# Performance work log

Measured on AMD Instinct MI355X. Metric: run time of the kernel, lower is better.

## Reference

```python
import jax, jax.numpy as jnp
import numpy as np


def setup_inputs() -> dict:
    key = jax.random.key(0)
    k_x, k_m, k_wq, k_wk, k_bq, k_bk = jax.random.split(key, 6)
    B, L, D, P = 8, 2048, 128, 64
    x = jax.random.normal(k_x, (B, L, D), dtype=jnp.float32)
    padding_mask = jax.random.randint(k_m, (B, L), 0, 2).astype(bool)
    lim = 1.0 / np.sqrt(D)
    Wq = jax.random.uniform(k_wq, (D, P), jnp.float32, -lim, lim)
    Wk = jax.random.uniform(k_wk, (D, P), jnp.float32, -lim, lim)
    bq = jax.random.uniform(k_bq, (P,), jnp.float32, -lim, lim)
    bk = jax.random.uniform(k_bk, (P,), jnp.float32, -lim, lim)
    return {"x": x, "padding_mask": padding_mask, "Wq": Wq, "bq": bq,
            "Wk": Wk, "bk": bk, "top_k": 64}


def reference(x, padding_mask, Wq, bq, Wk, bk, top_k):
    B, L, _ = x.shape
    P = Wq.shape[1]
    scale = jnp.asarray(P, x.dtype) ** 0.5
    Q = x @ Wq + bq                      # (B, L, P)
    K = x @ Wk + bk                      # (B, L, P)
    scores = jnp.einsum('blp,bmp->blm', Q, K) / scale   # (B, L, L)
    # valid pair mask: keep (i, j) only if both positions are unpadded
    full_mask = padding_mask[:, :, None] & padding_mask[:, None, :]
    flat = jnp.where(full_mask.reshape(B, L * L),
                     scores.reshape(B, L * L), -jnp.inf)
    topk_vals, topk_idx = jax.lax.top_k(flat, top_k)     # (B, K)
    topk_weights = jax.nn.softmax(topk_vals, axis=-1)
    topk_indices = jnp.stack([topk_idx // L, topk_idx % L], axis=-1)  # (B, K, 2)
    return topk_indices, topk_weights
```

## Files before the change

kernel.cpp:

```cpp
#include <hip/hip_runtime.h>
#include <float.h>
#include <limits.h>
#include <math.h>

namespace {

constexpr int NB = 8;
constexpr int SL = 2048;
constexpr int DIM = 128;
constexpr int PP = 64;
constexpr int KK = 64;
constexpr int ROWS = 128;
constexpr int CTILE = 128;
constexpr int NSTRIP = SL / ROWS;
constexpr int CSPLIT = 4;
constexpr int NSLOT = NSTRIP * CSPLIT;
constexpr int CAP = 512;
constexpr int PROJ_ROWS = 32;
constexpr int NPROJ = NB * SL / PROJ_ROWS;
constexpr float MARGIN = 4e-3f;

__device__ __forceinline__ bool cgt64(double v1, int i1, double v2, int i2) {
  return (v1 > v2) || (v1 == v2 && i1 < i2);
}
__device__ __forceinline__ bool cgt32(float v1, int i1, float v2, int i2) {
  return (v1 > v2) || (v1 == v2 && i1 < i2);
}

__global__ __launch_bounds__(256) void proj_compact_kernel(
    const float* __restrict__ x, const void* __restrict__ mask_raw,
    const float* __restrict__ Wq, const float* __restrict__ bq,
    const float* __restrict__ Wk, const float* __restrict__ bk,
    float* __restrict__ Q, float* __restrict__ K,
    int* __restrict__ pos, int* __restrict__ cnt) {
  const int tid = threadIdx.x;
  if (blockIdx.x >= NPROJ) {
    const int b = blockIdx.x - NPROJ;
    const int lane = tid & 63, wid = tid >> 6;
    __shared__ int bytemode;
    __shared__ int wsum[4];
    if (tid == 0) bytemode = 0;
    __syncthreads();
    const unsigned char* allb = (const unsigned char*)mask_raw;
    int local = 0;
    for (int t = tid; t < 512; t += 256)
      if ((t & 3) != 0 && allb[t] != 0) local = 1;
    if (local) atomicOr(&bytemode, 1);
    __syncthreads();
    int f[8]; int c = 0;
    const int base = tid * 8;
    if (bytemode) {
      const unsigned char* p = allb + (size_t)b * SL;
      for (int j = 0; j < 8; ++j) { f[j] = p[base + j] ? 1 : 0; c += f[j]; }
    } else {
      const int* p = (const int*)mask_raw + (size_t)b * SL;
      for (int j = 0; j < 8; ++j) { f[j] = p[base + j] ? 1 : 0; c += f[j]; }
    }
    int incl = c;
    for (int off = 1; off < 64; off <<= 1) {
      int t = __shfl_up(incl, off);
      if (lane >= off) incl += t;
    }
    if (lane == 63) wsum[wid] = incl;
    __syncthreads();
    int woff = 0;
    for (int w = 0; w < wid; ++w) woff += wsum[w];
    int k = woff + incl - c;
    for (int j = 0; j < 8; ++j)
      if (f[j]) pos[b * SL + (k++)] = base + j;
    if (tid == 255) cnt[b] = k;
    return;
  }
  __shared__ __align__(16) float sx[PROJ_ROWS * DIM];
  const int row0 = blockIdx.x * PROJ_ROWS;
  for (int t = tid; t < PROJ_ROWS * 32; t += 256) {
    const int row = t >> 5, f = t & 31;
    *(float4*)&sx[row * DIM + f * 4] =
        *(const float4*)(x + (size_t)(row0 + row) * DIM + f * 4);
  }
  __syncthreads();
  const int rq = tid >> 5;
  const int pp = (tid & 31) * 2;
  double aq[4][2] = {}, cq[4][2] = {}, ak[4][2] = {}, ck[4][2] = {};
  for (int d = 0; d < DIM; d += 4) {
    float4 xv[4];
#pragma unroll
    for (int i = 0; i < 4; ++i)
      xv[i] = *(const float4*)&sx[(rq * 4 + i) * DIM + d];
    const float2 wq0 = *(const float2*)&Wq[(d + 0) * PP + pp];
    const float2 wq1 = *(const float2*)&Wq[(d + 1) * PP + pp];
    const float2 wq2 = *(const float2*)&Wq[(d + 2) * PP + pp];
    const float2 wq3 = *(const float2*)&Wq[(d + 3) * PP + pp];
    const float2 wk0 = *(const float2*)&Wk[(d + 0) * PP + pp];
    const float2 wk1 = *(const float2*)&Wk[(d + 1) * PP + pp];
    const float2 wk2 = *(const float2*)&Wk[(d + 2) * PP + pp];
    const float2 wk3 = *(const float2*)&Wk[(d + 3) * PP + pp];
#pragma unroll
    for (int i = 0; i < 4; ++i) {
      const double x0 = (double)xv[i].x, x1 = (double)xv[i].y;
      const double x2 = (double)xv[i].z, x3 = (double)xv[i].w;
      aq[i][0] += x0 * (double)wq0.x; aq[i][1] += x0 * (double)wq0.y;
      cq[i][0] += x1 * (double)wq1.x; cq[i][1] += x1 * (double)wq1.y;
      aq[i][0] += x2 * (double)wq2.x; aq[i][1] += x2 * (double)wq2.y;
      cq[i][0] += x3 * (double)wq3.x; cq[i][1] += x3 * (double)wq3.y;
      ak[i][0] += x0 * (double)wk0.x; ak[i][1] += x0 * (double)wk0.y;
      ck[i][0] += x1 * (double)wk1.x; ck[i][1] += x1 * (double)wk1.y;
      ak[i][0] += x2 * (double)wk2.x; ak[i][1] += x2 * (double)wk2.y;
      ck[i][0] += x3 * (double)wk3.x; ck[i][1] += x3 * (double)wk3.y;
    }
  }
  const double b0q = (double)bq[pp], b1q = (double)bq[pp + 1];
  const double b0k = (double)bk[pp], b1k = (double)bk[pp + 1];
#pragma unroll
  for (int i = 0; i < 4; ++i) {
    const size_t o = ((size_t)row0 + rq * 4 + i) * PP + pp;
    Q[o]     = (float)(aq[i][0] + cq[i][0] + b0q);
    Q[o + 1] = (float)(aq[i][1] + cq[i][1] + b1q);
    K[o]     = (float)(ak[i][0] + ck[i][0] + b0k);
    K[o + 1] = (float)(ak[i][1] + ck[i][1] + b1k);
  }
}

__global__ __launch_bounds__(256, 2) void score_kernel(
    const float* __restrict__ Q, const float* __restrict__ K,
    const int* __restrict__ pos, const int* __restrict__ cnt,
    double* __restrict__ chunk_val, int* __restrict__ chunk_idx) {
  __shared__ __align__(16) float sQ[128 * 68];
  __shared__ __align__(16) float sK[128 * 68];
  __shared__ float cval[CAP];
  __shared__ int cidx[CAP];
  __shared__ float smax[256];
  __shared__ int spos_r[ROWS], spos_c[CTILE];
  __shared__ int cnt_sh, ovf, mcnt;
  __shared__ float thresh;

  const int b = blockIdx.y, strip = blockIdx.z, colq = blockIdx.x;
  const int tid = threadIdx.x, lane = tid & 63;
  const int nv = cnt[b];
  const int slot = (b * NSTRIP + strip) * CSPLIT + colq;
  const int r0 = strip * ROWS;
  const int per = (nv + CSPLIT - 1) / CSPLIT;
  const int cbeg = colq * per;
  const int cend = min(cbeg + per, nv);
  double* chv = chunk_val + (size_t)slot * KK;
  int* chi = chunk_idx + (size_t)slot * KK;
  if (r0 >= nv || cbeg >= cend) {
    if (tid < KK) { chv[tid] = -DBL_MAX; chi[tid] = INT_MAX; }
    return;
  }
  const int nrows = min(ROWS, nv - r0);
  if (tid < ROWS) spos_r[tid] = (tid < nrows) ? pos[b * SL + r0 + tid] : 0;
  for (int t = tid; t < 128 * 16; t += 256) {
    const int row = t >> 4, p4 = t & 15;
    float4 v = make_float4(0.f, 0.f, 0.f, 0.f);
    if (row < nrows) {
      const int g = pos[b * SL + r0 + row];
      v = *(const float4*)(Q + ((size_t)b * SL + g) * PP + p4 * 4);
    }
    *(float4*)&sQ[row * 68 + p4 * 4] = v;
  }
  if (tid == 0) { cnt_sh = 0; ovf = 0; thresh = -FLT_MAX; }
  __syncthreads();

  const int ry = tid & 15, cy = tid >> 4;

  for (int c0 = cbeg; c0 < cend; c0 += CTILE) {
    const int ncols = min(CTILE, cend - c0);
    if (tid < CTILE) spos_c[tid] = (tid < ncols) ? pos[b * SL + c0 + tid] : 0;
    for (int t = tid; t < 128 * 16; t += 256) {
      const int col = t >> 4, p4 = t & 15;
      float4 v = make_float4(0.f, 0.f, 0.f, 0.f);
      if (col < ncols) {
        const int g = pos[b * SL + c0 + col];
        v = *(const float4*)(K + ((size_t)b * SL + g) * PP + p4 * 4);
      }
      *(float4*)&sK[col * 68 + p4 * 4] = v;
    }
    __syncthreads();

    float acc[8][8] = {};
    for (int p4 = 0; p4 < 16; ++p4) {
      float4 qv[8], kv[8];
#pragma unroll
      for (int i = 0; i < 8; ++i) qv[i] = *(const float4*)&sQ[(ry + 16 * i) * 68 + p4 * 4];
#pragma unroll
      for (int j = 0; j < 8; ++j) kv[j] = *(const float4*)&sK[(cy + 16 * j) * 68 + p4 * 4];
#pragma unroll
      for (int i = 0; i < 8; ++i)
#pragma unroll
        for (int j = 0; j < 8; ++j) {
          acc[i][j] = fmaf(qv[i].x, kv[j].x, acc[i][j]);
          acc[i][j] = fmaf(qv[i].y, kv[j].y, acc[i][j]);
          acc[i][j] = fmaf(qv[i].z, kv[j].z, acc[i][j]);
          acc[i][j] = fmaf(qv[i].w, kv[j].w, acc[i][j]);
        }
    }

    if (c0 == cbeg) {
      float tmax = -FLT_MAX;
      for (int i = 0; i < 8; ++i) {
        const int rr = ry + 16 * i;
        if (rr >= nrows) continue;
        for (int j = 0; j < 8; ++j) {
          const int cc = cy + 16 * j;
          if (cc >= ncols) continue;
          tmax = fmaxf(tmax, acc[i][j] * 0.125f);
        }
      }
      smax[tid] = tmax;
      __syncthreads();
      for (int k2 = 2; k2 <= 256; k2 <<= 1)
        for (int j2 = k2 >> 1; j2 >= 1; j2 >>= 1) {
          if (tid < 128) {
            const int i = ((tid & ~(j2 - 1)) << 1) | (tid & (j2 - 1));
            const int p = i | j2;
            const bool desc = ((i & k2) == 0);
            const float vi = smax[i], vp = smax[p];
            const bool sw = desc ? (vp > vi) : (vi > vp);
            if (sw) { smax[i] = vp; smax[p] = vi; }
          }
          __syncthreads();
        }
      if (tid == 0 && smax[KK - 1] > -FLT_MAX) thresh = smax[KK - 1] - MARGIN;
      __syncthreads();
    }

    bool pushed = false;
    for (int attempt = 0; attempt < 8; ++attempt) {
      const float th = thresh;
      int nloc = 0;
      for (int i = 0; i < 8; ++i) {
        const int rr = ry + 16 * i;
        if (rr >= nrows) continue;
        for (int j = 0; j < 8; ++j) {
          const int cc = cy + 16 * j;
          if (cc >= ncols) continue;
          if (acc[i][j] * 0.125f >= th) nloc++;
        }
      }
      int incl = nloc;
      for (int off = 1; off < 64; off <<= 1) {
        int t2 = __shfl_up(incl, off);
        if (lane >= off) incl += t2;
      }
      const int wtot = __shfl(incl, 63);
      if (!pushed) {
        if (wtot == 0) {
          pushed = true;
        } else {
          int wbase = 0;
          if (lane == 63) {
            wbase = atomicAdd(&cnt_sh, wtot);
            if (wbase + wtot > CAP) { atomicAdd(&cnt_sh, -wtot); wbase = -1; ovf = 1; }
          }
          wbase = __shfl(wbase, 63);
          if (wbase >= 0) {
            int sl = wbase + incl - nloc;
            for (int i = 0; i < 8; ++i) {
              const int rr = ry + 16 * i;
              if (rr >= nrows) continue;
              for (int j = 0; j < 8; ++j) {
                const int cc = cy + 16 * j;
                if (cc >= ncols) continue;
                const float s = acc[i][j] * 0.125f;
                if (s >= th) {
                  cval[sl] = s;
                  cidx[sl] = spos_r[rr] * SL + spos_c[cc];
                  ++sl;
                }
              }
            }
            pushed = true;
          }
        }
      }
      __syncthreads();
      if (ovf == 0) break;
      {
        const int n = cnt_sh;
        for (int j = n + tid; j < CAP; j += 256) { cval[j] = -FLT_MAX; cidx[j] = INT_MAX; }
        __syncthreads();
        for (int k2 = 2; k2 <= CAP; k2 <<= 1)
          for (int j2 = k2 >> 1; j2 >= 1; j2 >>= 1) {
            const int i = ((tid & ~(j2 - 1)) << 1) | (tid & (j2 - 1));
            const int p = i | j2;
            const bool desc = ((i & k2) == 0);
            const float vi = cval[i], vp = cval[p];
            const int ii = cidx[i], ip = cidx[p];
            const bool sw = desc ? cgt32(vp, ip, vi, ii) : cgt32(vi, ii, vp, ip);
            if (sw) { cval[i] = vp; cidx[i] = ip; cval[p] = vi; cidx[p] = ii; }
            __syncthreads();
          }
        const float t64 = cval[KK - 1];
        const float nth = (t64 > -FLT_MAX) ? (t64 - MARGIN) : thresh;
        for (int j = tid; j < CAP; j += 256) {
          const bool in = (cidx[j] != INT_MAX) && (cval[j] >= nth);
          const bool nx = (j + 1 < CAP) && (cidx[j + 1] != INT_MAX) && (cval[j + 1] >= nth);
          if (in && !nx) mcnt = j + 1;
          if (j == 0 && !in) mcnt = 0;
        }
        __syncthreads();
        if (tid == 0) { thresh = nth; cnt_sh = mcnt; ovf = 0; }
        __syncthreads();
      }
    }
    __syncthreads();
  }

  const int n = cnt_sh;
  double* rval = (double*)sQ;
  for (int base2 = 0; base2 < n; base2 += 32) {
    const int s = base2 + (tid >> 3);
    double p = 0;
    if (s < n) {
      const int fi = cidx[s];
      const int orow = fi >> 11, ocol = fi & (SL - 1);
      const float* qr = Q + ((size_t)b * SL + orow) * PP + (tid & 7) * 8;
      const float* kr = K + ((size_t)b * SL + ocol) * PP + (tid & 7) * 8;
#pragma unroll
      for (int e = 0; e < 8; ++e) p = fma((double)qr[e], (double)kr[e], p);
    }
    p += __shfl_down(p, 4);
    p += __shfl_down(p, 2);
    p += __shfl_down(p, 1);
    if (((tid & 7) == 0) && s < n) rval[s] = p * 0.125;
  }
  int np2 = KK;
  while (np2 < n) np2 <<= 1;
  for (int j = n + tid; j < np2; j += 256) { rval[j] = -DBL_MAX; cidx[j] = INT_MAX; }
  __syncthreads();
  for (int k2 = 2; k2 <= np2; k2 <<= 1)
    for (int j2 = k2 >> 1; j2 >= 1; j2 >>= 1) {
      if (tid < (np2 >> 1)) {
        const int i = ((tid & ~(j2 - 1)) << 1) | (tid & (j2 - 1));
        const int p = i | j2;
        const bool desc = ((i & k2) == 0);
        const double vi = rval[i], vp = rval[p];
        const int ii = cidx[i], ip = cidx[p];
        const bool sw = desc ? cgt64(vp, ip, vi, ii) : cgt64(vi, ii, vp, ip);
        if (sw) { rval[i] = vp; cidx[i] = ip; rval[p] = vi; cidx[p] = ii; }
      }
      __syncthreads();
    }
  if (tid < KK) { chv[tid] = rval[tid]; chi[tid] = cidx[tid]; }
}

__global__ __launch_bounds__(256) void merge_kernel(
    const double* __restrict__ chunk_val, const int* __restrict__ chunk_idx,
    float* __restrict__ out) {
  __shared__ double sval[NSLOT * 16];
  __shared__ int sidx[NSLOT * 16];
  const int b = blockIdx.x, tid = threadIdx.x;
  const double* vb = chunk_val + (size_t)b * NSLOT * KK;
  const int* ib = chunk_idx + (size_t)b * NSLOT * KK;
  for (int t = tid; t < NSLOT * 16; t += 256) {
    const int list = t >> 4, e = t & 15;
    sval[t] = vb[list * KK + e];
    sidx[t] = ib[list * KK + e];
  }
  __syncthreads();
  if (tid < 64) {
    const int lane = tid;
    int hp = 0;
    double cur = sval[lane * 16];
    int curi = sidx[lane * 16];
    double myv = -DBL_MAX; int myi = INT_MAX;
    for (int k = 0; k < KK; ++k) {
      double bv = cur; int bi = curi; int bg = lane;
      for (int off2 = 32; off2 > 0; off2 >>= 1) {
        const double v2 = __shfl_down(bv, off2);
        const int i2 = __shfl_down(bi, off2);
        const int g2 = __shfl_down(bg, off2);
        if (cgt64(v2, i2, bv, bi)) { bv = v2; bi = i2; bg = g2; }
      }
      bv = __shfl(bv, 0); bi = __shfl(bi, 0); bg = __shfl(bg, 0);
      if (bg == lane) {
        const int h = ++hp;
        if (h < 16) { cur = sval[lane * 16 + h]; curi = sidx[lane * 16 + h]; }
        else if (h < KK) { cur = vb[lane * KK + h]; curi = ib[lane * KK + h]; }
        else { cur = -DBL_MAX; curi = INT_MAX; }
      }
      if (lane == k) { myv = bv; myi = bi; }
    }
    const double m = __shfl(myv, 0);
    double e = (myi == INT_MAX || myv == -DBL_MAX) ? 0.0 : exp(myv - m);
    double s = e;
    for (int off2 = 32; off2 > 0; off2 >>= 1) s += __shfl_down(s, off2);
    s = __shfl(s, 0);
    if (s <= 0.0) s = 1.0;
    const double w = e / s;
    int row = 0, col = 0;
    if (myi != INT_MAX) { row = myi >> 11; col = myi & (SL - 1); }
    float* oidx = out;
    float* owt = out + (size_t)NB * KK * 2;
    oidx[((size_t)b * KK + lane) * 2 + 0] = (float)row;
    oidx[((size_t)b * KK + lane) * 2 + 1] = (float)col;
    owt[(size_t)b * KK + lane] = (float)w;
  }
}

}

extern "C" void kernel_launch(void* const* d_in, const int* in_sizes, int n_in,
                              void* d_out, int out_size, void* d_ws, size_t ws_size,
                              hipStream_t stream) {
  const float* x = (const float*)d_in[0];
  const void* mask_raw = d_in[1];
  const float* Wq = (const float*)d_in[2];
  const float* bq = (const float*)d_in[3];
  const float* Wk = (const float*)d_in[4];
  const float* bk = (const float*)d_in[5];
  float* out = (float*)d_out;

  char* ws = (char*)d_ws;
  const size_t qk = (size_t)NB * SL * PP;
  float* Q = (float*)ws;
  float* K = (float*)(ws + qk * 4);
  size_t off = qk * 8;
  double* chunk_val = (double*)(ws + off); off += (size_t)NB * NSLOT * KK * 8;
  int* chunk_idx = (int*)(ws + off);       off += (size_t)NB * NSLOT * KK * 4;
  int* pos = (int*)(ws + off);             off += (size_t)NB * SL * 4;
  int* cntv = (int*)(ws + off);

  proj_compact_kernel<<<NPROJ + NB, 256, 0, stream>>>(
      x, mask_raw, Wq, bq, Wk, bk, Q, K, pos, cntv);
  score_kernel<<<dim3(CSPLIT, NB, NSTRIP), 256, 0, stream>>>(
      Q, K, pos, cntv, chunk_val, chunk_idx);
  merge_kernel<<<NB, 256, 0, stream>>>(chunk_val, chunk_idx, out);
}
```

Baseline: 191.9 us.

## Fuse projection, scoring and merge into one persistent kernel with atomic dependency counters

Merges the three kernel launches into a single launch whose block ranges play the projection, compaction, scoring and merge roles. Per-batch atomic counters with spin-waits replace the kernel boundaries, so scoring for one batch can start once that batch's projection is done, and the merge can start once its batch's scores are in. This removes launch gaps and lets stages overlap, at the cost of a memset launch, spin-wait polling, and a shared-memory union sized for the largest role, which may limit occupancy. Correctness relies on blocks being dispatched in index order so that the waiting blocks cannot starve the producers.

```diff
diff --git a/kernel.cpp b/kernel.cpp
--- a/kernel.cpp
+++ b/kernel.cpp
@@ -18,6 +18,8 @@
 constexpr int CAP = 512;
 constexpr int PROJ_ROWS = 32;
 constexpr int NPROJ = NB * SL / PROJ_ROWS;
+constexpr int NSCORE = CSPLIT * NB * NSTRIP;
+constexpr int PROJ_PER_BATCH = 64;
 constexpr float MARGIN = 4e-3f;
 
 __device__ __forceinline__ bool cgt64(double v1, int i1, double v2, int i2) {
@@ -27,29 +29,106 @@
   return (v1 > v2) || (v1 == v2 && i1 < i2);
 }
 
-__global__ __launch_bounds__(256) void proj_compact_kernel(
+union __align__(16) SMem {
+  struct {
+    float sQ[128 * 68];
+    float sK[128 * 68];
+    float cval[CAP];
+    int   cidx[CAP];
+    float smax[256];
+    int   spos_r[ROWS];
+    int   spos_c[CTILE];
+    int   cnt_sh, ovf, mcnt;
+    float thresh;
+  } sc;
+  struct { float sx[PROJ_ROWS * DIM]; } pj;
+  struct { int bytemode; int wsum[4]; } cp;
+  struct { double sval[NSLOT * 16]; int sidx[NSLOT * 16]; } mg;
+};
+
+__global__ __launch_bounds__(256, 2) void fused_kernel(
     const float* __restrict__ x, const void* __restrict__ mask_raw,
     const float* __restrict__ Wq, const float* __restrict__ bq,
     const float* __restrict__ Wk, const float* __restrict__ bk,
     float* __restrict__ Q, float* __restrict__ K,
-    int* __restrict__ pos, int* __restrict__ cnt) {
+    int* __restrict__ pos, int* __restrict__ cnt,
+    unsigned* __restrict__ ctr, unsigned* __restrict__ sdone,
+    double* __restrict__ chunk_val, int* __restrict__ chunk_idx,
+    float* __restrict__ out) {
+  __shared__ SMem sm;
+  const int bid = blockIdx.x;
   const int tid = threadIdx.x;
-  if (blockIdx.x >= NPROJ) {
-    const int b = blockIdx.x - NPROJ;
-    const int lane = tid & 63, wid = tid >> 6;
-    __shared__ int bytemode;
-    __shared__ int wsum[4];
-    if (tid == 0) bytemode = 0;
+  const int lane = tid & 63;
+
+  if (bid < NPROJ) {
+    float* sx = sm.pj.sx;
+    const int row0 = bid * PROJ_ROWS;
+    for (int t = tid; t < PROJ_ROWS * 32; t += 256) {
+      const int row = t >> 5, f = t & 31;
+      *(float4*)&sx[row * DIM + f * 4] =
+          *(const float4*)(x + (size_t)(row0 + row) * DIM + f * 4);
+    }
+    __syncthreads();
+    const int rq = tid >> 5;
+    const int pp = (tid & 31) * 2;
+    double aq[4][2] = {}, cq[4][2] = {}, ak[4][2] = {}, ck[4][2] = {};
+    for (int d = 0; d < DIM; d += 4) {
+      float4 xv[4];
+#pragma unroll
+      for (int i = 0; i < 4; ++i)
+        xv[i] = *(const float4*)&sx[(rq * 4 + i) * DIM + d];
+      const float2 wq0 = *(const float2*)&Wq[(d + 0) * PP + pp];
+      const float2 wq1 = *(const float2*)&Wq[(d + 1) * PP + pp];
+      const float2 wq2 = *(const float2*)&Wq[(d + 2) * PP + pp];
+      const float2 wq3 = *(const float2*)&Wq[(d + 3) * PP + pp];
+      const float2 wk0 = *(const float2*)&Wk[(d + 0) * PP + pp];
+      const float2 wk1 = *(const float2*)&Wk[(d + 1) * PP + pp];
+      const float2 wk2 = *(const float2*)&Wk[(d + 2) * PP + pp];
+      const float2 wk3 = *(const float2*)&Wk[(d + 3) * PP + pp];
+#pragma unroll
+      for (int i = 0; i < 4; ++i) {
+        const double x0 = (double)xv[i].x, x1 = (double)xv[i].y;
+        const double x2 = (double)xv[i].z, x3 = (double)xv[i].w;
+        aq[i][0] += x0 * (double)wq0.x; aq[i][1] += x0 * (double)wq0.y;
+        cq[i][0] += x1 * (double)wq1.x; cq[i][1] += x1 * (double)wq1.y;
+        aq[i][0] += x2 * (double)wq2.x; aq[i][1] += x2 * (double)wq2.y;
+        cq[i][0] += x3 * (double)wq3.x; cq[i][1] += x3 * (double)wq3.y;
+        ak[i][0] += x0 * (double)wk0.x; ak[i][1] += x0 * (double)wk0.y;
+        ck[i][0] += x1 * (double)wk1.x; ck[i][1] += x1 * (double)wk1.y;
+        ak[i][0] += x2 * (double)wk2.x; ak[i][1] += x2 * (double)wk2.y;
+        ck[i][0] += x3 * (double)wk3.x; ck[i][1] += x3 * (double)wk3.y;
+      }
+    }
+    const double b0q = (double)bq[pp], b1q = (double)bq[pp + 1];
+    const double b0k = (double)bk[pp], b1k = (double)bk[pp + 1];
+#pragma unroll
+    for (int i = 0; i < 4; ++i) {
+      const size_t o = ((size_t)row0 + rq * 4 + i) * PP + pp;
+      Q[o]     = (float)(aq[i][0] + cq[i][0] + b0q);
+      Q[o + 1] = (float)(aq[i][1] + cq[i][1] + b1q);
+      K[o]     = (float)(ak[i][0] + ck[i][0] + b0k);
+      K[o + 1] = (float)(ak[i][1] + ck[i][1] + b1k);
+    }
+    __threadfence();
+    __syncthreads();
+    if (tid == 0) atomicAdd(&ctr[bid >> 6], 1u);
+    return;
+  }
+
+  if (bid < NPROJ + NB) {
+    const int b = bid - NPROJ;
+    const int wid = tid >> 6;
+    if (tid == 0) sm.cp.bytemode = 0;
     __syncthreads();
     const unsigned char* allb = (const unsigned char*)mask_raw;
     int local = 0;
     for (int t = tid; t < 512; t += 256)
       if ((t & 3) != 0 && allb[t] != 0) local = 1;
-    if (local) atomicOr(&bytemode, 1);
+    if (local) atomicOr(&sm.cp.bytemode, 1);
     __syncthreads();
     int f[8]; int c = 0;
     const int base = tid * 8;
-    if (bytemode) {
+    if (sm.cp.bytemode) {
       const unsigned char* p = allb + (size_t)b * SL;
       for (int j = 0; j < 8; ++j) { f[j] = p[base + j] ? 1 : 0; c += f[j]; }
     } else {
@@ -61,341 +140,307 @@
       int t = __shfl_up(incl, off);
       if (lane >= off) incl += t;
     }
-    if (lane == 63) wsum[wid] = incl;
+    if (lane == 63) sm.cp.wsum[wid] = incl;
     __syncthreads();
     int woff = 0;
-    for (int w = 0; w < wid; ++w) woff += wsum[w];
+    for (int w = 0; w < wid; ++w) woff += sm.cp.wsum[w];
     int k = woff + incl - c;
     for (int j = 0; j < 8; ++j)
       if (f[j]) pos[b * SL + (k++)] = base + j;
     if (tid == 255) cnt[b] = k;
+    __threadfence();
+    __syncthreads();
+    if (tid == 0) atomicAdd(&ctr[b], 1u);
     return;
   }
-  __shared__ __align__(16) float sx[PROJ_ROWS * DIM];
-  const int row0 = blockIdx.x * PROJ_ROWS;
-  for (int t = tid; t < PROJ_ROWS * 32; t += 256) {
-    const int row = t >> 5, f = t & 31;
-    *(float4*)&sx[row * DIM + f * 4] =
-        *(const float4*)(x + (size_t)(row0 + row) * DIM + f * 4);
-  }
-  __syncthreads();
-  const int rq = tid >> 5;
-  const int pp = (tid & 31) * 2;
-  double aq[4][2] = {}, cq[4][2] = {}, ak[4][2] = {}, ck[4][2] = {};
-  for (int d = 0; d < DIM; d += 4) {
-    float4 xv[4];
-#pragma unroll
-    for (int i = 0; i < 4; ++i)
-      xv[i] = *(const float4*)&sx[(rq * 4 + i) * DIM + d];
-    const float2 wq0 = *(const float2*)&Wq[(d + 0) * PP + pp];
-    const float2 wq1 = *(const float2*)&Wq[(d + 1) * PP + pp];
-    const float2 wq2 = *(const float2*)&Wq[(d + 2) * PP + pp];
-    const float2 wq3 = *(const float2*)&Wq[(d + 3) * PP + pp];
-    const float2 wk0 = *(const float2*)&Wk[(d + 0) * PP + pp];
-    const float2 wk1 = *(const float2*)&Wk[(d + 1) * PP + pp];
-    const float2 wk2 = *(const float2*)&Wk[(d + 2) * PP + pp];
-    const float2 wk3 = *(const float2*)&Wk[(d + 3) * PP + pp];
-#pragma unroll
-    for (int i = 0; i < 4; ++i) {
-      const double x0 = (double)xv[i].x, x1 = (double)xv[i].y;
-      const double x2 = (double)xv[i].z, x3 = (double)xv[i].w;
-      aq[i][0] += x0 * (double)wq0.x; aq[i][1] += x0 * (double)wq0.y;
-      cq[i][0] += x1 * (double)wq1.x; cq[i][1] += x1 * (double)wq1.y;
-      aq[i][0] += x2 * (double)wq2.x; aq[i][1] += x2 * (double)wq2.y;
-      cq[i][0] += x3 * (double)wq3.x; cq[i][1] += x3 * (double)wq3.y;
-      ak[i][0] += x0 * (double)wk0.x; ak[i][1] += x0 * (double)wk0.y;
-      ck[i][0] += x1 * (double)wk1.x; ck[i][1] += x1 * (double)wk1.y;
-      ak[i][0] += x2 * (double)wk2.x; ak[i][1] += x2 * (double)wk2.y;
-      ck[i][0] += x3 * (double)wk3.x; ck[i][1] += x3 * (double)wk3.y;
-    }
-  }
-  const double b0q = (double)bq[pp], b1q = (double)bq[pp + 1];
-  const double b0k = (double)bk[pp], b1k = (double)bk[pp + 1];
-#pragma unroll
-  for (int i = 0; i < 4; ++i) {
-    const size_t o = ((size_t)row0 + rq * 4 + i) * PP + pp;
-    Q[o]     = (float)(aq[i][0] + cq[i][0] + b0q);
-    Q[o + 1] = (float)(aq[i][1] + cq[i][1] + b1q);
-    K[o]     = (float)(ak[i][0] + ck[i][0] + b0k);
-    K[o + 1] = (float)(ak[i][1] + ck[i][1] + b1k);
-  }
-}
-
-__global__ __launch_bounds__(256, 2) void score_kernel(
-    const float* __restrict__ Q, const float* __restrict__ K,
-    const int* __restrict__ pos, const int* __restrict__ cnt,
-    double* __restrict__ chunk_val, int* __restrict__ chunk_idx) {
-  __shared__ __align__(16) float sQ[128 * 68];
-  __shared__ __align__(16) float sK[128 * 68];
-  __shared__ float cval[CAP];
-  __shared__ int cidx[CAP];
-  __shared__ float smax[256];
-  __shared__ int spos_r[ROWS], spos_c[CTILE];
-  __shared__ int cnt_sh, ovf, mcnt;
-  __shared__ float thresh;
-
-  const int b = blockIdx.y, strip = blockIdx.z, colq = blockIdx.x;
-  const int tid = threadIdx.x, lane = tid & 63;
-  const int nv = cnt[b];
-  const int slot = (b * NSTRIP + strip) * CSPLIT + colq;
-  const int r0 = strip * ROWS;
-  const int per = (nv + CSPLIT - 1) / CSPLIT;
-  const int cbeg = colq * per;
-  const int cend = min(cbeg + per, nv);
-  double* chv = chunk_val + (size_t)slot * KK;
-  int* chi = chunk_idx + (size_t)slot * KK;
-  if (r0 >= nv || cbeg >= cend) {
-    if (tid < KK) { chv[tid] = -DBL_MAX; chi[tid] = INT_MAX; }
+
+  if (bid < NPROJ + NB + NSCORE) {
+    const int sid = bid - (NPROJ + NB);
+    const int colq = sid & 3;
+    const int b = (sid >> 2) & 7;
+    const int strip = sid >> 5;
+
+    if (tid == 0) {
+      while (atomicAdd(&ctr[b], 0u) < (unsigned)(PROJ_PER_BATCH + 1))
+        __builtin_amdgcn_s_sleep(8);
+    }
+    __syncthreads();
+    __threadfence();
+
+    float* sQ = sm.sc.sQ;
+    float* sK = sm.sc.sK;
+    const int nv = cnt[b];
+    const int slot = (b * NSTRIP + strip) * CSPLIT + colq;
+    const int r0 = strip * ROWS;
+    const int per = (nv + CSPLIT - 1) / CSPLIT;
+    const int cbeg = colq * per;
+    const int cend = min(cbeg + per, nv);
+    double* chv = chunk_val + (size_t)slot * KK;
+    int* chi = chunk_idx + (size_t)slot * KK;
+    if (r0 >= nv || cbeg >= cend) {
+      if (tid < KK) { chv[tid] = -DBL_MAX; chi[tid] = INT_MAX; }
+      __threadfence();
+      __syncthreads();
+      if (tid == 0) atomicAdd(&sdone[b], 1u);
+      return;
+    }
+    const int nrows = min(ROWS, nv - r0);
+    if (tid < ROWS) sm.sc.spos_r[tid] = (tid < nrows) ? pos[b * SL + r0 + tid] : 0;
+    for (int t = tid; t < 128 * 16; t += 256) {
+      const int row = t >> 4, p4 = t & 15;
+      float4 v = make_float4(0.f, 0.f, 0.f, 0.f);
+      if (row < nrows) {
+        const int g = pos[b * SL + r0 + row];
+        v = *(const float4*)(Q + ((size_t)b * SL + g) * PP + p4 * 4);
+      }
+      *(float4*)&sQ[row * 68 + p4 * 4] = v;
+    }
+    if (tid == 0) { sm.sc.cnt_sh = 0; sm.sc.ovf = 0; sm.sc.thresh = -FLT_MAX; }
+    __syncthreads();
+
+    const int ry = tid & 15, cy = tid >> 4;
+
+    for (int c0 = cbeg; c0 < cend; c0 += CTILE) {
+      const int ncols = min(CTILE, cend - c0);
+      if (tid < CTILE) sm.sc.spos_c[tid] = (tid < ncols) ? pos[b * SL + c0 + tid] : 0;
+      for (int t = tid; t < 128 * 16; t += 256) {
+        const int col = t >> 4, p4 = t & 15;
+        float4 v = make_float4(0.f, 0.f, 0.f, 0.f);
+        if (col < ncols) {
+          const int g = pos[b * SL + c0 + col];
+          v = *(const float4*)(K + ((size_t)b * SL + g) * PP + p4 * 4);
+        }
+        *(float4*)&sK[col * 68 + p4 * 4] = v;
+      }
+      __syncthreads();
+
+      float acc[8][8] = {};
+      for (int p4 = 0; p4 < 16; ++p4) {
+        float4 qv[8], kv[8];
+#pragma unroll
+        for (int i = 0; i < 8; ++i) qv[i] = *(const float4*)&sQ[(ry + 16 * i) * 68 + p4 * 4];
+#pragma unroll
+        for (int j = 0; j < 8; ++j) kv[j] = *(const float4*)&sK[(cy + 16 * j) * 68 + p4 * 4];
+#pragma unroll
+        for (int i = 0; i < 8; ++i)
+#pragma unroll
+          for (int j = 0; j < 8; ++j) {
+            acc[i][j] = fmaf(qv[i].x, kv[j].x, acc[i][j]);
+            acc[i][j] = fmaf(qv[i].y, kv[j].y, acc[i][j]);
+            acc[i][j] = fmaf(qv[i].z, kv[j].z, acc[i][j]);
+            acc[i][j] = fmaf(qv[i].w, kv[j].w, acc[i][j]);
+          }
+      }
+
+      if (c0 == cbeg) {
+        float tmax = -FLT_MAX;
+        for (int i = 0; i < 8; ++i) {
+          const int rr = ry + 16 * i;
+          if (rr >= nrows) continue;
+          for (int j = 0; j < 8; ++j) {
+            const int cc = cy + 16 * j;
+            if (cc >= ncols) continue;
+            tmax = fmaxf(tmax, acc[i][j] * 0.125f);
+          }
+        }
+        sm.sc.smax[tid] = tmax;
+        __syncthreads();
+        for (int k2 = 2; k2 <= 256; k2 <<= 1)
+          for (int j2 = k2 >> 1; j2 >= 1; j2 >>= 1) {
+            if (tid < 128) {
+              const int i = ((tid & ~(j2 - 1)) << 1) | (tid & (j2 - 1));
+              const int p = i | j2;
+              const bool desc = ((i & k2) == 0);
+              const float vi = sm.sc.smax[i], vp = sm.sc.smax[p];
+              const bool sw = desc ? (vp > vi) : (vi > vp);
+              if (sw) { sm.sc.smax[i] = vp; sm.sc.smax[p] = vi; }
+            }
+            __syncthreads();
+          }
+        if (tid == 0 && sm.sc.smax[KK - 1] > -FLT_MAX)
+          sm.sc.thresh = sm.sc.smax[KK - 1] - MARGIN;
+        __syncthreads();
+      }
+
+      bool pushed = false;
+      for (int attempt = 0; attempt < 8; ++attempt) {
+        const float th = sm.sc.thresh;
+        int nloc = 0;
+        for (int i = 0; i < 8; ++i) {
+          const int rr = ry + 16 * i;
+          if (rr >= nrows) continue;
+          for (int j = 0; j < 8; ++j) {
+            const int cc = cy + 16 * j;
+            if (cc >= ncols) continue;
+            if (acc[i][j] * 0.125f >= th) nloc++;
+          }
+        }
+        int incl = nloc;
+        for (int off = 1; off < 64; off <<= 1) {
+          int t2 = __shfl_up(incl, off);
+          if (lane >= off) incl += t2;
+        }
+        const int wtot = __shfl(incl, 63);
+        if (!pushed) {
+          if (wtot == 0) {
+            pushed = true;
+          } else {
+            int wbase = 0;
+            if (lane == 63) {
+              wbase = atomicAdd(&sm.sc.cnt_sh, wtot);
+              if (wbase + wtot > CAP) { atomicAdd(&sm.sc.cnt_sh, -wtot); wbase = -1; sm.sc.ovf = 1; }
+            }
+            wbase = __shfl(wbase, 63);
+            if (wbase >= 0) {
+              int sl = wbase + incl - nloc;
+              for (int i = 0; i < 8; ++i) {
+                const int rr = ry + 16 * i;
+                if (rr >= nrows) continue;
+                for (int j = 0; j < 8; ++j) {
+                  const int cc = cy + 16 * j;
+                  if (cc >= ncols) continue;
+                  const float s = acc[i][j] * 0.125f;
+                  if (s >= th) {
+                    sm.sc.cval[sl] = s;
+                    sm.sc.cidx[sl] = sm.sc.spos_r[rr] * SL + sm.sc.spos_c[cc];
+                    ++sl;
+                  }
+                }
+              }
+              pushed = true;
+            }
+          }
+        }
+        __syncthreads();
+        if (sm.sc.ovf == 0) break;
+        {
+          const int n = sm.sc.cnt_sh;
+          for (int j = n + tid; j < CAP; j += 256) { sm.sc.cval[j] = -FLT_MAX; sm.sc.cidx[j] = INT_MAX; }
+          __syncthreads();
+          for (int k2 = 2; k2 <= CAP; k2 <<= 1)
+            for (int j2 = k2 >> 1; j2 >= 1; j2 >>= 1) {
+              const int i = ((tid & ~(j2 - 1)) << 1) | (tid & (j2 - 1));
+              const int p = i | j2;
+              const bool desc = ((i & k2) == 0);
+              const float vi = sm.sc.cval[i], vp = sm.sc.cval[p];
+              const int ii = sm.sc.cidx[i], ip = sm.sc.cidx[p];
+              const bool sw = desc ? cgt32(vp, ip, vi, ii) : cgt32(vi, ii, vp, ip);
+              if (sw) { sm.sc.cval[i] = vp; sm.sc.cidx[i] = ip; sm.sc.cval[p] = vi; sm.sc.cidx[p] = ii; }
+              __syncthreads();
+            }
+          const float t64 = sm.sc.cval[KK - 1];
+          const float nth = (t64 > -FLT_MAX) ? (t64 - MARGIN) : sm.sc.thresh;
+          for (int j = tid; j < CAP; j += 256) {
+            const bool in = (sm.sc.cidx[j] != INT_MAX) && (sm.sc.cval[j] >= nth);
+            const bool nx = (j + 1 < CAP) && (sm.sc.cidx[j + 1] != INT_MAX) && (sm.sc.cval[j + 1] >= nth);
+            if (in && !nx) sm.sc.mcnt = j + 1;
+            if (j == 0 && !in) sm.sc.mcnt = 0;
+          }
+          __syncthreads();
+          if (tid == 0) { sm.sc.thresh = nth; sm.sc.cnt_sh = sm.sc.mcnt; sm.sc.ovf = 0; }
+          __syncthreads();
+        }
+      }
+      __syncthreads();
+    }
+
+    const int n = sm.sc.cnt_sh;
+    double* rval = (double*)sQ;
+    for (int base2 = 0; base2 < n; base2 += 32) {
+      const int s = base2 + (tid >> 3);
+      double p = 0;
+      if (s < n) {
+        const int fi = sm.sc.cidx[s];
+        const int orow = fi >> 11, ocol = fi & (SL - 1);
+        const float* qr = Q + ((size_t)b * SL + orow) * PP + (tid & 7) * 8;
+        const float* kr = K + ((size_t)b * SL + ocol) * PP + (tid & 7) * 8;
+#pragma unroll
+        for (int e = 0; e < 8; ++e) p = fma((double)qr[e], (double)kr[e], p);
+      }
+      p += __shfl_down(p, 4);
+      p += __shfl_down(p, 2);
+      p += __shfl_down(p, 1);
+      if (((tid & 7) == 0) && s < n) rval[s] = p * 0.125;
+    }
+    int np2 = KK;
+    while (np2 < n) np2 <<= 1;
+    for (int j = n + tid; j < np2; j += 256) { rval[j] = -DBL_MAX; sm.sc.cidx[j] = INT_MAX; }
+    __syncthreads();
+    for (int k2 = 2; k2 <= np2; k2 <<= 1)
+      for (int j2 = k2 >> 1; j2 >= 1; j2 >>= 1) {
+        if (tid < (np2 >> 1)) {
+          const int i = ((tid & ~(j2 - 1)) << 1) | (tid & (j2 - 1));
+          const int p = i | j2;
+          const bool desc = ((i & k2) == 0);
+          const double vi = rval[i], vp = rval[p];
+          const int ii = sm.sc.cidx[i], ip = sm.sc.cidx[p];
+          const bool sw = desc ? cgt64(vp, ip, vi, ii) : cgt64(vi, ii, vp, ip);
+          if (sw) { rval[i] = vp; sm.sc.cidx[i] = ip; rval[p] = vi; sm.sc.cidx[p] = ii; }
+        }
+        __syncthreads();
+      }
+    if (tid < KK) { chv[tid] = rval[tid]; chi[tid] = sm.sc.cidx[tid]; }
+    __threadfence();
+    __syncthreads();
+    if (tid == 0) atomicAdd(&sdone[b], 1u);
     return;
   }
-  const int nrows = min(ROWS, nv - r0);
-  if (tid < ROWS) spos_r[tid] = (tid < nrows) ? pos[b * SL + r0 + tid] : 0;
-  for (int t = tid; t < 128 * 16; t += 256) {
-    const int row = t >> 4, p4 = t & 15;
-    float4 v = make_float4(0.f, 0.f, 0.f, 0.f);
-    if (row < nrows) {
-      const int g = pos[b * SL + r0 + row];
-      v = *(const float4*)(Q + ((size_t)b * SL + g) * PP + p4 * 4);
-    }
-    *(float4*)&sQ[row * 68 + p4 * 4] = v;
-  }
-  if (tid == 0) { cnt_sh = 0; ovf = 0; thresh = -FLT_MAX; }
-  __syncthreads();
-
-  const int ry = tid & 15, cy = tid >> 4;
-
-  for (int c0 = cbeg; c0 < cend; c0 += CTILE) {
-    const int ncols = min(CTILE, cend - c0);
-    if (tid < CTILE) spos_c[tid] = (tid < ncols) ? pos[b * SL + c0 + tid] : 0;
-    for (int t = tid; t < 128 * 16; t += 256) {
-      const int col = t >> 4, p4 = t & 15;
-      float4 v = make_float4(0.f, 0.f, 0.f, 0.f);
-      if (col < ncols) {
-        const int g = pos[b * SL + c0 + col];
-        v = *(const float4*)(K + ((size_t)b * SL + g) * PP + p4 * 4);
-      }
-      *(float4*)&sK[col * 68 + p4 * 4] = v;
-    }
-    __syncthreads();
-
-    float acc[8][8] = {};
-    for (int p4 = 0; p4 < 16; ++p4) {
-      float4 qv[8], kv[8];
-#pragma unroll
-      for (int i = 0; i < 8; ++i) qv[i] = *(const float4*)&sQ[(ry + 16 * i) * 68 + p4 * 4];
-#pragma unroll
-      for (int j = 0; j < 8; ++j) kv[j] = *(const float4*)&sK[(cy + 16 * j) * 68 + p4 * 4];
-#pragma unroll
-      for (int i = 0; i < 8; ++i)
-#pragma unroll
-        for (int j = 0; j < 8; ++j) {
-          acc[i][j] = fmaf(qv[i].x, kv[j].x, acc[i][j]);
-          acc[i][j] = fmaf(qv[i].y, kv[j].y, acc[i][j]);
-          acc[i][j] = fmaf(qv[i].z, kv[j].z, acc[i][j]);
-          acc[i][j] = fmaf(qv[i].w, kv[j].w, acc[i][j]);
-        }
-    }
-
-    if (c0 == cbeg) {
-      float tmax = -FLT_MAX;
-      for (int i = 0; i < 8; ++i) {
-        const int rr = ry + 16 * i;
-        if (rr >= nrows) continue;
-        for (int j = 0; j < 8; ++j) {
-          const int cc = cy + 16 * j;
-          if (cc >= ncols) continue;
-          tmax = fmaxf(tmax, acc[i][j] * 0.125f);
-        }
-      }
-      smax[tid] = tmax;
-      __syncthreads();
-      for (int k2 = 2; k2 <= 256; k2 <<= 1)
-        for (int j2 = k2 >> 1; j2 >= 1; j2 >>= 1) {
-          if (tid < 128) {
-            const int i = ((tid & ~(j2 - 1)) << 1) | (tid & (j2 - 1));
-            const int p = i | j2;
-            const bool desc = ((i & k2) == 0);
-            const float vi = smax[i], vp = smax[p];
-            const bool sw = desc ? (vp > vi) : (vi > vp);
-            if (sw) { smax[i] = vp; smax[p] = vi; }
-          }
-          __syncthreads();
-        }
-      if (tid == 0 && smax[KK - 1] > -FLT_MAX) thresh = smax[KK - 1] - MARGIN;
-      __syncthreads();
-    }
-
-    bool pushed = false;
-    for (int attempt = 0; attempt < 8; ++attempt) {
-      const float th = thresh;
-      int nloc = 0;
-      for (int i = 0; i < 8; ++i) {
-        const int rr = ry + 16 * i;
-        if (rr >= nrows) continue;
-        for (int j = 0; j < 8; ++j) {
-          const int cc = cy + 16 * j;
-          if (cc >= ncols) continue;
-          if (acc[i][j] * 0.125f >= th) nloc++;
-        }
-      }
-      int incl = nloc;
-      for (int off = 1; off < 64; off <<= 1) {
-        int t2 = __shfl_up(incl, off);
-        if (lane >= off) incl += t2;
-      }
-      const int wtot = __shfl(incl, 63);
-      if (!pushed) {
-        if (wtot == 0) {
-          pushed = true;
-        } else {
-          int wbase = 0;
-          if (lane == 63) {
-            wbase = atomicAdd(&cnt_sh, wtot);
-            if (wbase + wtot > CAP) { atomicAdd(&cnt_sh, -wtot); wbase = -1; ovf = 1; }
-          }
-          wbase = __shfl(wbase, 63);
-          if (wbase >= 0) {
-            int sl = wbase + incl - nloc;
-            for (int i = 0; i < 8; ++i) {
-              const int rr = ry + 16 * i;
-              if (rr >= nrows) continue;
-              for (int j = 0; j < 8; ++j) {
-                const int cc = cy + 16 * j;
-                if (cc >= ncols) continue;
-                const float s = acc[i][j] * 0.125f;
-                if (s >= th) {
-                  cval[sl] = s;
-                  cidx[sl] = spos_r[rr] * SL + spos_c[cc];
-                  ++sl;
-                }
-              }
-            }
-            pushed = true;
-          }
-        }
-      }
-      __syncthreads();
-      if (ovf == 0) break;
-      {
-        const int n = cnt_sh;
-        for (int j = n + tid; j < CAP; j += 256) { cval[j] = -FLT_MAX; cidx[j] = INT_MAX; }
-        __syncthreads();
-        for (int k2 = 2; k2 <= CAP; k2 <<= 1)
-          for (int j2 = k2 >> 1; j2 >= 1; j2 >>= 1) {
-            const int i = ((tid & ~(j2 - 1)) << 1) | (tid & (j2 - 1));
-            const int p = i | j2;
-            const bool desc = ((i & k2) == 0);
-            const float vi = cval[i], vp = cval[p];
-            const int ii = cidx[i], ip = cidx[p];
-            const bool sw = desc ? cgt32(vp, ip, vi, ii) : cgt32(vi, ii, vp, ip);
-            if (sw) { cval[i] = vp; cidx[i] = ip; cval[p] = vi; cidx[p] = ii; }
-            __syncthreads();
-          }
-        const float t64 = cval[KK - 1];
-        const float nth = (t64 > -FLT_MAX) ? (t64 - MARGIN) : thresh;
-        for (int j = tid; j < CAP; j += 256) {
-          const bool in = (cidx[j] != INT_MAX) && (cval[j] >= nth);
-          const bool nx = (j + 1 < CAP) && (cidx[j + 1] != INT_MAX) && (cval[j + 1] >= nth);
-          if (in && !nx) mcnt = j + 1;
-          if (j == 0 && !in) mcnt = 0;
-        }
-        __syncthreads();
-        if (tid == 0) { thresh = nth; cnt_sh = mcnt; ovf = 0; }
-        __syncthreads();
-      }
-    }
-    __syncthreads();
-  }
-
-  const int n = cnt_sh;
-  double* rval = (double*)sQ;
-  for (int base2 = 0; base2 < n; base2 += 32) {
-    const int s = base2 + (tid >> 3);
-    double p = 0;
-    if (s < n) {
-      const int fi = cidx[s];
-      const int orow = fi >> 11, ocol = fi & (SL - 1);
-      const float* qr = Q + ((size_t)b * SL + orow) * PP + (tid & 7) * 8;
-      const float* kr = K + ((size_t)b * SL + ocol) * PP + (tid & 7) * 8;
-#pragma unroll
-      for (int e = 0; e < 8; ++e) p = fma((double)qr[e], (double)kr[e], p);
-    }
-    p += __shfl_down(p, 4);
-    p += __shfl_down(p, 2);
-    p += __shfl_down(p, 1);
-    if (((tid & 7) == 0) && s < n) rval[s] = p * 0.125;
-  }
-  int np2 = KK;
-  while (np2 < n) np2 <<= 1;
-  for (int j = n + tid; j < np2; j += 256) { rval[j] = -DBL_MAX; cidx[j] = INT_MAX; }
-  __syncthreads();
-  for (int k2 = 2; k2 <= np2; k2 <<= 1)
-    for (int j2 = k2 >> 1; j2 >= 1; j2 >>= 1) {
-      if (tid < (np2 >> 1)) {
-        const int i = ((tid & ~(j2 - 1)) << 1) | (tid & (j2 - 1));
-        const int p = i | j2;
-        const bool desc = ((i & k2) == 0);
-        const double vi = rval[i], vp = rval[p];
-        const int ii = cidx[i], ip = cidx[p];
-        const bool sw = desc ? cgt64(vp, ip, vi, ii) : cgt64(vi, ii, vp, ip);
-        if (sw) { rval[i] = vp; cidx[i] = ip; rval[p] = vi; cidx[p] = ii; }
-      }
-      __syncthreads();
-    }
-  if (tid < KK) { chv[tid] = rval[tid]; chi[tid] = cidx[tid]; }
-}
-
-__global__ __launch_bounds__(256) void merge_kernel(
-    const double* __restrict__ chunk_val, const int* __restrict__ chunk_idx,
-    float* __restrict__ out) {
-  __shared__ double sval[NSLOT * 16];
-  __shared__ int sidx[NSLOT * 16];
-  const int b = blockIdx.x, tid = threadIdx.x;
-  const double* vb = chunk_val + (size_t)b * NSLOT * KK;
-  const int* ib = chunk_idx + (size_t)b * NSLOT * KK;
-  for (int t = tid; t < NSLOT * 16; t += 256) {
-    const int list = t >> 4, e = t & 15;
-    sval[t] = vb[list * KK + e];
-    sidx[t] = ib[list * KK + e];
-  }
-  __syncthreads();
-  if (tid < 64) {
-    const int lane = tid;
-    int hp = 0;
-    double cur = sval[lane * 16];
-    int curi = sidx[lane * 16];
-    double myv = -DBL_MAX; int myi = INT_MAX;
-    for (int k = 0; k < KK; ++k) {
-      double bv = cur; int bi = curi; int bg = lane;
-      for (int off2 = 32; off2 > 0; off2 >>= 1) {
-        const double v2 = __shfl_down(bv, off2);
-        const int i2 = __shfl_down(bi, off2);
-        const int g2 = __shfl_down(bg, off2);
-        if (cgt64(v2, i2, bv, bi)) { bv = v2; bi = i2; bg = g2; }
-      }
-      bv = __shfl(bv, 0); bi = __shfl(bi, 0); bg = __shfl(bg, 0);
-      if (bg == lane) {
-        const int h = ++hp;
-        if (h < 16) { cur = sval[lane * 16 + h]; curi = sidx[lane * 16 + h]; }
-        else if (h < KK) { cur = vb[lane * KK + h]; curi = ib[lane * KK + h]; }
-        else { cur = -DBL_MAX; curi = INT_MAX; }
-      }
-      if (lane == k) { myv = bv; myi = bi; }
-    }
-    const double m = __shfl(myv, 0);
-    double e = (myi == INT_MAX || myv == -DBL_MAX) ? 0.0 : exp(myv - m);
-    double s = e;
-    for (int off2 = 32; off2 > 0; off2 >>= 1) s += __shfl_down(s, off2);
-    s = __shfl(s, 0);
-    if (s <= 0.0) s = 1.0;
-    const double w = e / s;
-    int row = 0, col = 0;
-    if (myi != INT_MAX) { row = myi >> 11; col = myi & (SL - 1); }
-    float* oidx = out;
-    float* owt = out + (size_t)NB * KK * 2;
-    oidx[((size_t)b * KK + lane) * 2 + 0] = (float)row;
-    oidx[((size_t)b * KK + lane) * 2 + 1] = (float)col;
-    owt[(size_t)b * KK + lane] = (float)w;
+
+  {
+    const int b = bid - (NPROJ + NB + NSCORE);
+    if (tid == 0) {
+      while (atomicAdd(&sdone[b], 0u) < (unsigned)NSLOT)
+        __builtin_amdgcn_s_sleep(8);
+    }
+    __syncthreads();
+    __threadfence();
+
+    const double* vb = chunk_val + (size_t)b * NSLOT * KK;
+    const int* ib = chunk_idx + (size_t)b * NSLOT * KK;
+    for (int t = tid; t < NSLOT * 16; t += 256) {
+      const int list = t >> 4, e = t & 15;
+      sm.mg.sval[t] = vb[list * KK + e];
+      sm.mg.sidx[t] = ib[list * KK + e];
+    }
+    __syncthreads();
+    if (tid < 64) {
+      const int ln = tid;
+      int hp = 0;
+      double cur = sm.mg.sval[ln * 16];
+      int curi = sm.mg.sidx[ln * 16];
+      double myv = -DBL_MAX; int myi = INT_MAX;
+      for (int k = 0; k < KK; ++k) {
+        double bv = cur; int bi = curi; int bg = ln;
+        for (int off2 = 32; off2 > 0; off2 >>= 1) {
+          const double v2 = __shfl_down(bv, off2);
+          const int i2 = __shfl_down(bi, off2);
+          const int g2 = __shfl_down(bg, off2);
+          if (cgt64(v2, i2, bv, bi)) { bv = v2; bi = i2; bg = g2; }
+        }
+        bv = __shfl(bv, 0); bi = __shfl(bi, 0); bg = __shfl(bg, 0);
+        if (bg == ln) {
+          const int h = ++hp;
+          if (h < 16) { cur = sm.mg.sval[ln * 16 + h]; curi = sm.mg.sidx[ln * 16 + h]; }
+          else if (h < KK) { cur = vb[ln * KK + h]; curi = ib[ln * KK + h]; }
+          else { cur = -DBL_MAX; curi = INT_MAX; }
+        }
+        if (ln == k) { myv = bv; myi = bi; }
+      }
+      const double m = __shfl(myv, 0);
+      double e = (myi == INT_MAX || myv == -DBL_MAX) ? 0.0 : exp(myv - m);
+      double s = e;
+      for (int off2 = 32; off2 > 0; off2 >>= 1) s += __shfl_down(s, off2);
+      s = __shfl(s, 0);
+      if (s <= 0.0) s = 1.0;
+      const double w = e / s;
+      int row = 0, col = 0;
+      if (myi != INT_MAX) { row = myi >> 11; col = myi & (SL - 1); }
+      float* oidx = out;
+      float* owt = out + (size_t)NB * KK * 2;
+      oidx[((size_t)b * KK + ln) * 2 + 0] = (float)row;
+      oidx[((size_t)b * KK + ln) * 2 + 1] = (float)col;
+      owt[(size_t)b * KK + ln] = (float)w;
+    }
   }
 }
 
@@ -420,11 +465,13 @@
   double* chunk_val = (double*)(ws + off); off += (size_t)NB * NSLOT * KK * 8;
   int* chunk_idx = (int*)(ws + off);       off += (size_t)NB * NSLOT * KK * 4;
   int* pos = (int*)(ws + off);             off += (size_t)NB * SL * 4;
-  int* cntv = (int*)(ws + off);
-
-  proj_compact_kernel<<<NPROJ + NB, 256, 0, stream>>>(
-      x, mask_raw, Wq, bq, Wk, bk, Q, K, pos, cntv);
-  score_kernel<<<dim3(CSPLIT, NB, NSTRIP), 256, 0, stream>>>(
-      Q, K, pos, cntv, chunk_val, chunk_idx);
-  merge_kernel<<<NB, 256, 0, stream>>>(chunk_val, chunk_idx, out);
+  int* cntv = (int*)(ws + off);            off += NB * sizeof(int);
+  unsigned* ctr = (unsigned*)(ws + off);   off += NB * sizeof(unsigned);
+  unsigned* sdone = (unsigned*)(ws + off);
+
+  hipMemsetAsync(ctr, 0, 2 * NB * sizeof(unsigned), stream);
+
+  fused_kernel<<<NPROJ + NB + NSCORE + NB, 256, 0, stream>>>(
+      x, mask_raw, Wq, bq, Wk, bk, Q, K, pos, cntv, ctr, sdone,
+      chunk_val, chunk_idx, out);
 }
```

After: 316.8 us. 1.65x slower.
